# Optimization experiments

Hardware: AMD Instinct MI355X
Metric: run time of the kernel (lower is better)

The kernel has to match this reference:

```python
import jax, jax.numpy as jnp
import numpy as np

B, C, H, W = 32, 256, 32, 32
D = max(16, C // 4)  # 64
K = 8


def setup_inputs() -> dict:
    key = jax.random.key(0)
    ks = jax.random.split(key, 4)
    x = jax.random.normal(ks[0], (B, C, H, W), dtype=jnp.float32)
    wq = jax.random.normal(ks[1], (D, C), dtype=jnp.float32) * (1.0 / np.sqrt(C))
    wk = jax.random.normal(ks[2], (D, C), dtype=jnp.float32) * (1.0 / np.sqrt(C))
    wv = jax.random.normal(ks[3], (C, C), dtype=jnp.float32) * (1.0 / np.sqrt(C))
    bq = jnp.zeros((D,), dtype=jnp.float32)
    bk = jnp.zeros((D,), dtype=jnp.float32)
    bv = jnp.zeros((C,), dtype=jnp.float32)
    scale = jnp.ones((1,), dtype=jnp.float32)
    return {"x": x, "wq": wq, "bq": bq, "wk": wk, "bk": bk, "wv": wv, "bv": bv, "scale": scale}


def reference(x, wq, bq, wk, bk, wv, bv, scale):
    b, c, h, w = x.shape
    n = h * w
    xf = x.reshape(b, c, n)                      # [B,C,N]
    # 1x1 convs are pointwise GEMMs over the channel dim
    q = jnp.einsum('dc,bcn->bdn', wq, xf) + bq[None, :, None]   # [B,D,N]
    k = jnp.einsum('dc,bcn->bdn', wk, xf) + bk[None, :, None]   # [B,D,N]
    v = jnp.einsum('ec,bcn->ben', wv, xf) + bv[None, :, None]   # [B,C,N]
    d = q.shape[1]
    sim = jnp.einsum('bdn,bdm->bnm', q, k) / jnp.sqrt(jnp.float32(d))  # [B,N,N]
    sim = sim - 1e9 * jnp.eye(n, dtype=sim.dtype)[None]          # mask self
    topk_val, topk_idx = jax.lax.top_k(sim, K)                    # [B,N,K]
    weights = jax.nn.softmax(topk_val, axis=-1)                   # [B,N,K]
    v_t = v.transpose(0, 2, 1)                                    # [B,N,C]
    gathered = v_t[jnp.arange(b)[:, None, None], topk_idx]        # [B,N,K,C]
    out = jnp.einsum('bnk,bnkc->bnc', weights, gathered)          # [B,N,C]
    out = out.transpose(0, 2, 1).reshape(b, c, h, w)
    return x + scale * out
```

## Files before the change

kernel.cpp:

```cpp
#include <hip/hip_runtime.h>

#define B_ 32
#define C_ 256
#define N_ 1024
#define D_ 64

__device__ __forceinline__ unsigned long long pack_key(float v, int m) {
    const unsigned int bits = __float_as_uint(v);
    const unsigned int mono = (bits & 0x80000000u) ? ~bits : (bits | 0x80000000u);
    return ((unsigned long long)mono << 10) | (unsigned long long)(1023 - m);
}

template <int CTRL>
__device__ __forceinline__ float dpp_mov_f(float x) {
    return __int_as_float(__builtin_amdgcn_update_dpp(
        0, __float_as_int(x), CTRL, 0xF, 0xF, true));
}
#define DPP_QUAD_XOR1   0xB1
#define DPP_QUAD_XOR2   0x4E
#define DPP_HALF_MIRROR 0x141
#define DPP_ROW_ROR8    0x128

__global__ __launch_bounds__(384) void wt_kernel(
    const float* __restrict__ wq, const float* __restrict__ wk,
    const float* __restrict__ wv, float* __restrict__ wt)
{
    const int c = blockIdx.x;
    const int r = threadIdx.x;
    float v;
    if      (r < 64)  v = wq[(size_t)r * C_ + c];
    else if (r < 128) v = wk[(size_t)(r - 64) * C_ + c];
    else              v = wv[(size_t)(r - 128) * C_ + c];
    wt[(size_t)c * 384 + r] = v;
}

__global__ __launch_bounds__(256) void proj_kernel(
    const float* __restrict__ x, const float* __restrict__ wt,
    const float* __restrict__ bq, const float* __restrict__ bk,
    const float* __restrict__ bv,
    float* __restrict__ qk, float* __restrict__ vt)
{
    const int lid = blockIdx.x;
    const int b     = (lid & 7) + 8 * (lid / 384);
    const int inner = (lid >> 3) % 48;
    const int rg    = inner % 12;
    const int nt    = inner / 12;
    const int r0 = rg * 32;
    const int n0 = nt * 256;
    const int lane = threadIdx.x & 63;
    const int wu = __builtin_amdgcn_readfirstlane(threadIdx.x >> 6);
    const int rw = r0 + wu * 8;

    float acc[8][4];
    #pragma unroll
    for (int i = 0; i < 8; ++i)
        #pragma unroll
        for (int j = 0; j < 4; ++j) acc[i][j] = 0.f;

    const float* xp = x + (size_t)b * C_ * N_ + n0 + lane * 4;
    const float* wp = wt + rw;

    #pragma unroll 8
    for (int c = 0; c < C_; ++c) {
        const float4 xv = *(const float4*)(xp + (size_t)c * N_);
        const float* wr = wp + (size_t)c * 384;
        const float4 w0 = *(const float4*)(wr);
        const float4 w1 = *(const float4*)(wr + 4);
        const float wv8[8] = { w0.x, w0.y, w0.z, w0.w, w1.x, w1.y, w1.z, w1.w };
        #pragma unroll
        for (int i = 0; i < 8; ++i) {
            acc[i][0] = fmaf(wv8[i], xv.x, acc[i][0]);
            acc[i][1] = fmaf(wv8[i], xv.y, acc[i][1]);
            acc[i][2] = fmaf(wv8[i], xv.z, acc[i][2]);
            acc[i][3] = fmaf(wv8[i], xv.w, acc[i][3]);
        }
    }

    if (r0 < 128) {
        #pragma unroll
        for (int i = 0; i < 8; ++i) {
            const int R = rw + i;
            const float bb = (R < 64) ? bq[R] : bk[R - 64];
            float4 o; o.x = acc[i][0]+bb; o.y = acc[i][1]+bb; o.z = acc[i][2]+bb; o.w = acc[i][3]+bb;
            *(float4*)&qk[((size_t)b * 128 + R) * N_ + n0 + lane * 4] = o;
        }
    } else {
        const int e0 = rw - 128;
        float be[8];
        #pragma unroll
        for (int i = 0; i < 8; ++i) be[i] = bv[e0 + i];
        #pragma unroll
        for (int j = 0; j < 4; ++j) {
            const int n = n0 + lane * 4 + j;
            float* dst = &vt[((size_t)b * N_ + n) * C_ + e0];
            float4 o0; o0.x = acc[0][j]+be[0]; o0.y = acc[1][j]+be[1]; o0.z = acc[2][j]+be[2]; o0.w = acc[3][j]+be[3];
            float4 o1; o1.x = acc[4][j]+be[4]; o1.y = acc[5][j]+be[5]; o1.z = acc[6][j]+be[6]; o1.w = acc[7][j]+be[7];
            *(float4*)dst       = o0;
            *(float4*)(dst + 4) = o1;
        }
    }
}

__global__ __launch_bounds__(512) void attn_kernel(
    const float* __restrict__ x,
    const float* __restrict__ qk,
    const float* __restrict__ vt,
    const float* __restrict__ scale,
    float* __restrict__ out)
{
    const int lid = blockIdx.x;
    const int b  = (lid & 7) + 8 * (lid >> 9);
    const int n0 = ((lid >> 3) & 63) * 16;
    const int t  = threadIdx.x;
    const int lane = t & 63;
    const int w  = t >> 6;
    const int ms = w & 3;
    const int rg = __builtin_amdgcn_readfirstlane(t >> 8);

    __shared__ unsigned long long cand[16][196];
    __shared__ int   ccnt[16][4];

    const int m_base = ms * 256 + lane * 4;

    float a0[8], a1[8], a2[8], a3[8];
    #pragma unroll
    for (int r = 0; r < 8; ++r) { a0[r]=0.f; a1[r]=0.f; a2[r]=0.f; a3[r]=0.f; }

    const float* kb = qk + ((size_t)b * 128 + 64) * N_ + m_base;
    const float* qb = qk + (size_t)b * 128 * N_ + n0 + rg * 8;

    #pragma unroll 2
    for (int d0 = 0; d0 < D_; d0 += 4) {
        const float4 k0 = *(const float4*)&kb[(size_t)(d0+0) * N_];
        const float4 k1 = *(const float4*)&kb[(size_t)(d0+1) * N_];
        const float4 k2 = *(const float4*)&kb[(size_t)(d0+2) * N_];
        const float4 k3 = *(const float4*)&kb[(size_t)(d0+3) * N_];

        float qs[4][8];
        #pragma unroll
        for (int dd = 0; dd < 4; ++dd) {
            #pragma unroll
            for (int rq = 0; rq < 2; ++rq) {
                const float4 qv = *(const float4*)&qb[(size_t)(d0 + dd) * N_ + rq * 4];
                qs[dd][rq*4+0] = qv.x; qs[dd][rq*4+1] = qv.y;
                qs[dd][rq*4+2] = qv.z; qs[dd][rq*4+3] = qv.w;
            }
        }

        #pragma unroll
        for (int r = 0; r < 8; ++r) {
            a0[r] = fmaf(qs[0][r], k0.x, a0[r]); a0[r] = fmaf(qs[1][r], k1.x, a0[r]);
            a0[r] = fmaf(qs[2][r], k2.x, a0[r]); a0[r] = fmaf(qs[3][r], k3.x, a0[r]);
            a1[r] = fmaf(qs[0][r], k0.y, a1[r]); a1[r] = fmaf(qs[1][r], k1.y, a1[r]);
            a1[r] = fmaf(qs[2][r], k2.y, a1[r]); a1[r] = fmaf(qs[3][r], k3.y, a1[r]);
            a2[r] = fmaf(qs[0][r], k0.z, a2[r]); a2[r] = fmaf(qs[1][r], k1.z, a2[r]);
            a2[r] = fmaf(qs[2][r], k2.z, a2[r]); a2[r] = fmaf(qs[3][r], k3.z, a2[r]);
            a3[r] = fmaf(qs[0][r], k0.w, a3[r]); a3[r] = fmaf(qs[1][r], k1.w, a3[r]);
            a3[r] = fmaf(qs[2][r], k2.w, a3[r]); a3[r] = fmaf(qs[3][r], k3.w, a3[r]);
        }
    }

    const unsigned long long lt = (1ull << lane) - 1ull;
    #pragma unroll
    for (int r = 0; r < 8; ++r) {
        const int ri = rg * 8 + r;
        const int nrow = n0 + ri;
        float t0 = a0[r], t1 = a1[r], t2 = a2[r], t3 = a3[r];
        const int dj = nrow - m_base;
        if      (dj == 0) t0 = -1.0e9f;
        else if (dj == 1) t1 = -1.0e9f;
        else if (dj == 2) t2 = -1.0e9f;
        else if (dj == 3) t3 = -1.0e9f;

        float lm = fmaxf(fmaxf(t0, t1), fmaxf(t2, t3));
        lm = fmaxf(lm, dpp_mov_f<DPP_QUAD_XOR1>(lm));
        lm = fmaxf(lm, dpp_mov_f<DPP_QUAD_XOR2>(lm));
        lm = fmaxf(lm, dpp_mov_f<DPP_HALF_MIRROR>(lm));
        float Th = fminf(lm, dpp_mov_f<DPP_ROW_ROR8>(lm));
        Th = fminf(Th, __shfl_xor(Th, 16));
        Th = fminf(Th, __shfl_xor(Th, 32));

        int cnt = 0;
        {
            const bool p = (t0 >= Th);
            const unsigned long long msk = __ballot(p);
            const int pos = cnt + (int)__popcll(msk & lt);
            if (p && pos < 48) cand[ri][ms * 49 + pos] = pack_key(t0, m_base + 0);
            cnt += (int)__popcll(msk);
        }
        {
            const bool p = (t1 >= Th);
            const unsigned long long msk = __ballot(p);
            const int pos = cnt + (int)__popcll(msk & lt);
            if (p && pos < 48) cand[ri][ms * 49 + pos] = pack_key(t1, m_base + 1);
            cnt += (int)__popcll(msk);
        }
        {
            const bool p = (t2 >= Th);
            const unsigned long long msk = __ballot(p);
            const int pos = cnt + (int)__popcll(msk & lt);
            if (p && pos < 48) cand[ri][ms * 49 + pos] = pack_key(t2, m_base + 2);
            cnt += (int)__popcll(msk);
        }
        {
            const bool p = (t3 >= Th);
            const unsigned long long msk = __ballot(p);
            const int pos = cnt + (int)__popcll(msk & lt);
            if (p && pos < 48) cand[ri][ms * 49 + pos] = pack_key(t3, m_base + 3);
            cnt += (int)__popcll(msk);
        }

        if (cnt > 48) {
            unsigned long long K0 = pack_key(t0, m_base + 0);
            unsigned long long K1 = pack_key(t1, m_base + 1);
            unsigned long long K2 = pack_key(t2, m_base + 2);
            unsigned long long K3 = pack_key(t3, m_base + 3);
            #pragma unroll 1
            for (int round = 0; round < 8; ++round) {
                unsigned long long kl = K0 > K1 ? K0 : K1;
                kl = K2 > kl ? K2 : kl;
                kl = K3 > kl ? K3 : kl;
                #pragma unroll
                for (int off = 32; off >= 1; off >>= 1) {
                    const unsigned long long ks = __shfl_xor(kl, off);
                    if (ks > kl) kl = ks;
                }
                if (lane == 0) cand[ri][ms * 49 + round] = kl;
                if      (K0 == kl) K0 = 0ull;
                else if (K1 == kl) K1 = 0ull;
                else if (K2 == kl) K2 = 0ull;
                else if (K3 == kl) K3 = 0ull;
            }
            cnt = 8;
        }
        if (lane == 0) ccnt[ri][ms] = cnt;
    }
    __syncthreads();

    const float* vtb = vt + (size_t)b * N_ * C_;
    #pragma unroll
    for (int rr = 0; rr < 2; ++rr) {
        const int r = w * 2 + rr;
        const int seg = lane >> 4;
        const int i0  = lane & 15;
        const int cn  = ccnt[r][seg];
        unsigned long long k0 = (i0      < cn) ? cand[r][seg * 49 + i0     ] : 0ull;
        unsigned long long k1 = (i0 + 16 < cn) ? cand[r][seg * 49 + i0 + 16] : 0ull;
        unsigned long long k2 = (i0 + 32 < cn) ? cand[r][seg * 49 + i0 + 32] : 0ull;

        float ev[8]; unsigned int mi[8];
        float S = 0.f, vmax = 0.f;
        #pragma unroll
        for (int round = 0; round < 8; ++round) {
            unsigned long long km = k0 > k1 ? k0 : k1;
            km = k2 > km ? k2 : km;
            #pragma unroll
            for (int off = 32; off >= 1; off >>= 1) {
                const unsigned long long ks = __shfl_xor(km, off);
                if (ks > km) km = ks;
            }
            const unsigned int mono = (unsigned int)(km >> 10);
            mi[round] = 1023u - ((unsigned int)km & 1023u);
            const unsigned int bits = (mono & 0x80000000u) ? (mono & 0x7FFFFFFFu) : ~mono;
            const float vraw = __uint_as_float(bits);
            if (round == 0) vmax = vraw;
            const float e = __expf((vraw - vmax) * 0.125f);
            S += e;
            ev[round] = e;
            if (k0 == km) k0 = 0ull;
            if (k1 == km) k1 = 0ull;
            if (k2 == km) k2 = 0ull;
        }

        float4 o = make_float4(0.f, 0.f, 0.f, 0.f);
        #pragma unroll
        for (int round = 0; round < 8; ++round) {
            const float4 vv = *(const float4*)&vtb[(size_t)mi[round] * C_ + lane * 4];
            o.x += ev[round] * vv.x; o.y += ev[round] * vv.y;
            o.z += ev[round] * vv.z; o.w += ev[round] * vv.w;
        }
        const float inv = 1.f / S;
        float* orow = (float*)&cand[r][0];
        *(float4*)&orow[lane * 4] = make_float4(o.x*inv, o.y*inv, o.z*inv, o.w*inv);
    }
    __syncthreads();

    const float sc = scale[0];
    const float* xb = x + (size_t)b * C_ * N_;
    float* ob = out + (size_t)b * C_ * N_;
    const int nl = t & 15;
    const int cg = t >> 4;
    const float* orow = (const float*)&cand[nl][0];
    #pragma unroll
    for (int i = 0; i < 8; ++i) {
        const int cc = i * 32 + cg;
        const size_t gi = (size_t)cc * N_ + n0 + nl;
        ob[gi] = xb[gi] + sc * orow[cc];
    }
}

extern "C" void kernel_launch(void* const* d_in, const int* in_sizes, int n_in,
                              void* d_out, int out_size, void* d_ws, size_t ws_size,
                              hipStream_t stream) {
    const float* x     = (const float*)d_in[0];
    const float* wq    = (const float*)d_in[1];
    const float* bq    = (const float*)d_in[2];
    const float* wk    = (const float*)d_in[3];
    const float* bk    = (const float*)d_in[4];
    const float* wv    = (const float*)d_in[5];
    const float* bv    = (const float*)d_in[6];
    const float* scale = (const float*)d_in[7];
    float* out = (float*)d_out;

    float* qk = (float*)d_ws;
    float* vt = qk + (size_t)B_ * 128 * N_;
    float* wt = vt + (size_t)B_ * N_ * C_;

    wt_kernel<<<dim3(256), 384, 0, stream>>>(wq, wk, wv, wt);
    proj_kernel<<<dim3(1536), 256, 0, stream>>>(x, wt, bq, bk, bv, qk, vt);
    attn_kernel<<<dim3(2048), 512, 0, stream>>>(x, qk, vt, scale, out);
}
```

Baseline: 190.5 us.

## Compute V projection with bf16 MFMA via transposed bf16 x staging

```diff
diff --git a/kernel.cpp b/kernel.cpp
--- a/kernel.cpp
+++ b/kernel.cpp
@@ -1,10 +1,14 @@
 #include <hip/hip_runtime.h>
+#include <hip/hip_bf16.h>
 
 #define B_ 32
 #define C_ 256
 #define N_ 1024
 #define D_ 64
 
+typedef __attribute__((ext_vector_type(8))) short bf16x8;
+typedef __attribute__((ext_vector_type(4))) float f32x4;
+
 __device__ __forceinline__ unsigned long long pack_key(float v, int m) {
     const unsigned int bits = __float_as_uint(v);
     const unsigned int mono = (bits & 0x80000000u) ? ~bits : (bits | 0x80000000u);
@@ -21,9 +25,15 @@
 #define DPP_HALF_MIRROR 0x141
 #define DPP_ROW_ROR8    0x128
 
+__device__ __forceinline__ unsigned short f2bf(float f) {
+    __hip_bfloat16 h = __float2bfloat16(f);
+    return *(unsigned short*)&h;
+}
+
 __global__ __launch_bounds__(384) void wt_kernel(
     const float* __restrict__ wq, const float* __restrict__ wk,
-    const float* __restrict__ wv, float* __restrict__ wt)
+    const float* __restrict__ wv, float* __restrict__ wt,
+    unsigned short* __restrict__ wvb, int do_wvb)
 {
     const int c = blockIdx.x;
     const int r = threadIdx.x;
@@ -32,9 +42,154 @@
     else if (r < 128) v = wk[(size_t)(r - 64) * C_ + c];
     else              v = wv[(size_t)(r - 128) * C_ + c];
     wt[(size_t)c * 384 + r] = v;
-}
-
-__global__ __launch_bounds__(256) void proj_kernel(
+    if (do_wvb && r >= 128) {
+        const int e = c, cc = r - 128;
+        wvb[(size_t)e * C_ + cc] = f2bf(wv[(size_t)e * C_ + cc]);
+    }
+}
+
+__global__ __launch_bounds__(256) void xt_kernel(
+    const float* __restrict__ x, unsigned short* __restrict__ xtb)
+{
+    const int lid = blockIdx.x;
+    const int b     = (lid & 7) + 8 * (lid >> 9);
+    const int inner = (lid >> 3) & 63;
+    const int nt    = inner & 15;
+    const int ct    = inner >> 4;
+    const int n0 = nt * 64, c0 = ct * 64;
+    const int t  = threadIdx.x;
+
+    __shared__ __align__(16) float tl[64][65];
+
+    const float* xb = x + (size_t)b * C_ * N_;
+    #pragma unroll
+    for (int p = 0; p < 4; ++p) {
+        const int cl = (t >> 4) + p * 16;
+        const int nl = (t & 15) * 4;
+        *(float4*)&tl[cl][nl] = *(const float4*)&xb[(size_t)(c0 + cl) * N_ + n0 + nl];
+    }
+    __syncthreads();
+
+    unsigned short* dstb = xtb + ((size_t)b * N_) * C_;
+    #pragma unroll
+    for (int p = 0; p < 4; ++p) {
+        const int nl = (t >> 4) + p * 16;
+        const int cl = (t & 15) * 4;
+        ushort4 o;
+        o.x = f2bf(tl[cl + 0][nl]);
+        o.y = f2bf(tl[cl + 1][nl]);
+        o.z = f2bf(tl[cl + 2][nl]);
+        o.w = f2bf(tl[cl + 3][nl]);
+        *(ushort4*)&dstb[(size_t)(n0 + nl) * C_ + c0 + cl] = o;
+    }
+}
+
+__global__ __launch_bounds__(256) void projqk_kernel(
+    const float* __restrict__ x, const float* __restrict__ wt,
+    const float* __restrict__ bq, const float* __restrict__ bk,
+    float* __restrict__ qk)
+{
+    const int lid = blockIdx.x;
+    const int b     = (lid & 7) + 8 * (lid >> 8);
+    const int inner = (lid >> 3) & 31;
+    const int rg    = inner & 7;
+    const int nt    = inner >> 3;
+    const int r0 = rg * 16;
+    const int n0 = nt * 256;
+    const int lane = threadIdx.x & 63;
+    const int wu = __builtin_amdgcn_readfirstlane(threadIdx.x >> 6);
+    const int rw = r0 + wu * 4;
+
+    float acc[4][4];
+    #pragma unroll
+    for (int i = 0; i < 4; ++i)
+        #pragma unroll
+        for (int j = 0; j < 4; ++j) acc[i][j] = 0.f;
+
+    const float* xp = x + (size_t)b * C_ * N_ + n0 + lane * 4;
+    const float* wp = wt + rw;
+
+    #pragma unroll 8
+    for (int c = 0; c < C_; ++c) {
+        const float4 xv = *(const float4*)(xp + (size_t)c * N_);
+        const float4 w0 = *(const float4*)(wp + (size_t)c * 384);
+        const float wv4[4] = { w0.x, w0.y, w0.z, w0.w };
+        #pragma unroll
+        for (int i = 0; i < 4; ++i) {
+            acc[i][0] = fmaf(wv4[i], xv.x, acc[i][0]);
+            acc[i][1] = fmaf(wv4[i], xv.y, acc[i][1]);
+            acc[i][2] = fmaf(wv4[i], xv.z, acc[i][2]);
+            acc[i][3] = fmaf(wv4[i], xv.w, acc[i][3]);
+        }
+    }
+
+    #pragma unroll
+    for (int i = 0; i < 4; ++i) {
+        const int R = rw + i;
+        const float bb = (R < 64) ? bq[R] : bk[R - 64];
+        float4 o; o.x = acc[i][0]+bb; o.y = acc[i][1]+bb; o.z = acc[i][2]+bb; o.w = acc[i][3]+bb;
+        *(float4*)&qk[((size_t)b * 128 + R) * N_ + n0 + lane * 4] = o;
+    }
+}
+
+__global__ __launch_bounds__(256) void vmfma_kernel(
+    const unsigned short* __restrict__ xtb, const unsigned short* __restrict__ wvb,
+    const float* __restrict__ bv, float* __restrict__ vt)
+{
+    const int lid = blockIdx.x;
+    const int b     = (lid & 7) + 8 * (lid >> 9);
+    const int inner = (lid >> 3) & 63;
+    const int nb    = inner & 15;
+    const int eb    = inner >> 4;
+    const int t  = threadIdx.x;
+    const int lane = t & 63;
+    const int w  = t >> 6;
+    const int n_base = nb * 64 + (w & 1) * 32;
+    const int e_base = eb * 64 + (w >> 1) * 32;
+
+    const int l16  = lane & 15;
+    const int koff = 8 * (lane >> 4);
+
+    f32x4 acc[2][2];
+    #pragma unroll
+    for (int i = 0; i < 2; ++i)
+        #pragma unroll
+        for (int j = 0; j < 2; ++j) acc[i][j] = (f32x4)(0.f);
+
+    const unsigned short* ab = wvb + (size_t)(e_base + l16) * C_ + koff;
+    const unsigned short* bb = xtb + ((size_t)b * N_ + n_base + l16) * C_ + koff;
+
+    #pragma unroll
+    for (int kk = 0; kk < 8; ++kk) {
+        const int c0 = kk * 32;
+        bf16x8 a0 = *(const bf16x8*)(ab + c0);
+        bf16x8 a1 = *(const bf16x8*)(ab + 16 * C_ + c0);
+        bf16x8 b0 = *(const bf16x8*)(bb + c0);
+        bf16x8 b1 = *(const bf16x8*)(bb + 16 * C_ + c0);
+        acc[0][0] = __builtin_amdgcn_mfma_f32_16x16x32_bf16(a0, b0, acc[0][0], 0, 0, 0);
+        acc[0][1] = __builtin_amdgcn_mfma_f32_16x16x32_bf16(a0, b1, acc[0][1], 0, 0, 0);
+        acc[1][0] = __builtin_amdgcn_mfma_f32_16x16x32_bf16(a1, b0, acc[1][0], 0, 0, 0);
+        acc[1][1] = __builtin_amdgcn_mfma_f32_16x16x32_bf16(a1, b1, acc[1][1], 0, 0, 0);
+    }
+
+    const int col  = lane & 15;
+    const int row0 = (lane >> 4) * 4;
+    #pragma unroll
+    for (int i = 0; i < 2; ++i) {
+        const int e0 = e_base + i * 16 + row0;
+        const float4 bvv = *(const float4*)&bv[e0];
+        #pragma unroll
+        for (int j = 0; j < 2; ++j) {
+            const int n = n_base + j * 16 + col;
+            float4 o;
+            o.x = acc[i][j][0] + bvv.x; o.y = acc[i][j][1] + bvv.y;
+            o.z = acc[i][j][2] + bvv.z; o.w = acc[i][j][3] + bvv.w;
+            *(float4*)&vt[((size_t)b * N_ + n) * C_ + e0] = o;
+        }
+    }
+}
+
+__global__ __launch_bounds__(256) void proj_full_kernel(
     const float* __restrict__ x, const float* __restrict__ wt,
     const float* __restrict__ bq, const float* __restrict__ bk,
     const float* __restrict__ bv,
@@ -315,8 +470,19 @@
     float* qk = (float*)d_ws;
     float* vt = qk + (size_t)B_ * 128 * N_;
     float* wt = vt + (size_t)B_ * N_ * C_;
-
-    wt_kernel<<<dim3(256), 384, 0, stream>>>(wq, wk, wv, wt);
-    proj_kernel<<<dim3(1536), 256, 0, stream>>>(x, wt, bq, bk, bv, qk, vt);
+    unsigned short* wvb = (unsigned short*)(wt + 256 * 384);
+    unsigned short* xtb = wvb + (size_t)C_ * C_;
+
+    const size_t needed = ((char*)(xtb + (size_t)B_ * N_ * C_)) - (char*)d_ws;
+    const int mfma_path = (ws_size >= needed) ? 1 : 0;
+
+    wt_kernel<<<dim3(256), 384, 0, stream>>>(wq, wk, wv, wt, wvb, mfma_path);
+    if (mfma_path) {
+        xt_kernel<<<dim3(2048), 256, 0, stream>>>(x, xtb);
+        projqk_kernel<<<dim3(1024), 256, 0, stream>>>(x, wt, bq, bk, qk);
+        vmfma_kernel<<<dim3(2048), 256, 0, stream>>>(xtb, wvb, bv, vt);
+    } else {
+        proj_full_kernel<<<dim3(1536), 256, 0, stream>>>(x, wt, bq, bk, bv, qk, vt);
+    }
     attn_kernel<<<dim3(2048), 512, 0, stream>>>(x, qk, vt, scale, out);
 }
```

New measurement: 187.7 us. About the same (-1.5%).
